# Kernel optimization log

Hardware: AMD Instinct MI355X
Metric: run time of the kernel (lower is better)

## Reference

```python
import jax, jax.numpy as jnp
import numpy as np

B, T, D_IN, H, NH, R = 32, 1024, 64, 128, 4, 3
HD = H // NH  # 32


def _p(key, shape, scale=0.02):
    return jax.random.normal(key, shape, dtype=jnp.float32) * scale


def setup_inputs() -> dict:
    key = jax.random.key(0)
    ks = jax.random.split(key, 8)
    return {
        "x": jax.random.normal(ks[0], (B, T, D_IN), dtype=jnp.float32),
        "theta_w": _p(ks[1], (H, D_IN)),
        "theta_b": jnp.zeros((H,), jnp.float32),
        "in_proj_w": _p(ks[2], (3 * H, H)),
        "in_proj_b": jnp.zeros((3 * H,), jnp.float32),
        "out_proj_w": _p(ks[3], (H, H)),
        "out_proj_b": jnp.zeros((H,), jnp.float32),
        "ln_g": jnp.ones((H,), jnp.float32),
        "ln_b": jnp.zeros((H,), jnp.float32),
        "w1": _p(ks[4], (H, H)),
        "b1": jnp.zeros((H,), jnp.float32),
        "w2": _p(ks[5], (2, H)),
        "b2": jnp.zeros((2,), jnp.float32),
    }


def _build_adj(t, radius):
    # banded adjacency: adj[i,j] = 1/(1+|i-j|) for |i-j| <= radius, row-normalized
    idx = jnp.arange(t)
    d = jnp.abs(idx[:, None] - idx[None, :])
    adj = jnp.where(d <= radius, 1.0 / (1.0 + d.astype(jnp.float32)), 0.0)
    return adj / jnp.clip(adj.sum(axis=1, keepdims=True), 1e-8)


def reference(x, theta_w, theta_b, in_proj_w, in_proj_b, out_proj_w, out_proj_b,
              ln_g, ln_b, w1, b1, w2, b2):
    h = x @ theta_w.T + theta_b                       # [B,T,H]
    adj = _build_adj(T, R)                            # [T,T]
    g = jnp.einsum('ij,bjh->bih', adj, h)             # banded temporal aggregation

    # torch nn.MultiheadAttention (batch_first, eval -> no dropout)
    qkv = g @ in_proj_w.T + in_proj_b                 # [B,T,3H]
    q, k, v = jnp.split(qkv, 3, axis=-1)
    split_heads = lambda t: t.reshape(B, T, NH, HD).transpose(0, 2, 1, 3)
    q, k, v = split_heads(q), split_heads(k), split_heads(v)
    scores = jnp.einsum('bntd,bnsd->bnts', q, k) / jnp.sqrt(jnp.float32(HD))
    attn = jax.nn.softmax(scores, axis=-1)
    o = jnp.einsum('bnts,bnsd->bntd', attn, v)
    o = o.transpose(0, 2, 1, 3).reshape(B, T, H)
    a = o @ out_proj_w.T + out_proj_b                 # [B,T,H]

    # head on last timestep: LayerNorm -> Linear -> GELU(exact) -> Linear
    last = a[:, -1, :]                                # [B,H]
    mu = last.mean(-1, keepdims=True)
    var = ((last - mu) ** 2).mean(-1, keepdims=True)
    ln = (last - mu) / jnp.sqrt(var + 1e-5) * ln_g + ln_b
    hid = jax.nn.gelu(ln @ w1.T + b1, approximate=False)
    return hid @ w2.T + b2                            # [B,2]
```

## Files before the change

### kernel.cpp

```cpp
#include <hip/hip_runtime.h>
#include <math.h>

#define TT 1024

__global__ __launch_bounds__(1024) void k_bn(
    const float* __restrict__ x, const float* __restrict__ theta_w,
    const float* __restrict__ theta_b, const float* __restrict__ ipw,
    const float* __restrict__ ipb, float* __restrict__ u_ws) {
  const int bid = blockIdx.x;
  const int b = bid & 31;
  const int n = bid >> 5;
  const int tid = threadIdx.x;

  __shared__ float s_xs[64];
  __shared__ float s_y[128];
  __shared__ float s_qn[32];
  __shared__ float s_z[128];
  __shared__ __align__(16) float s_r[64];
  __shared__ __align__(16) float s_t[TT];
  __shared__ __align__(16) float s_p[TT];
  __shared__ __align__(16) float s_pt[TT];
  __shared__ float s_up[16][64];
  __shared__ float s_red[16];

  const float* __restrict__ xb = x + (size_t)b * TT * 64;

  if (tid < 64) {
    float acc = xb[(TT - 1) * 64 + tid]
              + 0.5f        * xb[(TT - 2) * 64 + tid]
              + (1.f / 3.f) * xb[(TT - 3) * 64 + tid]
              + 0.25f       * xb[(TT - 4) * 64 + tid];
    s_xs[tid] = acc * (12.f / 25.f);
  }
  __syncthreads();
  if (tid < 128) {
    const float* tr = theta_w + tid * 64;
    float acc = theta_b[tid];
    for (int d = 0; d < 64; ++d) acc += tr[d] * s_xs[d];
    s_y[tid] = acc;
  }
  __syncthreads();
  if (tid < 512) {
    const int g = tid >> 4, l = tid & 15;
    const int e = n * 32 + g;
    const float* wr = ipw + e * 128 + l * 8;
    float acc = 0.f;
    #pragma unroll
    for (int u = 0; u < 8; ++u) acc += wr[u] * s_y[l * 8 + u];
    acc += __shfl_xor(acc, 1);
    acc += __shfl_xor(acc, 2);
    acc += __shfl_xor(acc, 4);
    acc += __shfl_xor(acc, 8);
    if (l == 0) s_qn[g] = acc + ipb[e];
  }
  __syncthreads();
  if (tid < 128) {
    const int c = tid;
    float acc = 0.f;
    for (int e = 0; e < 32; ++e)
      acc += ipw[(128 + n * 32 + e) * 128 + c] * s_qn[e];
    s_z[c] = acc;
  }
  __syncthreads();
  if (tid < 64) {
    const int d = tid;
    float acc = 0.f;
    for (int c = 0; c < 128; ++c) acc += theta_w[c * 64 + d] * s_z[c];
    s_r[d] = acc * 0.17677669529663687f;
  }
  __syncthreads();

  {
    const int g = tid >> 4, l = tid & 15;
    const float4 rv = ((const float4*)s_r)[l];
    for (int it = 0; it < 16; ++it) {
      const int j = it * 64 + g;
      const float4 xv = ((const float4*)(xb + j * 64))[l];
      float p = xv.x * rv.x + xv.y * rv.y + xv.z * rv.z + xv.w * rv.w;
      #pragma unroll
      for (int m = 1; m <= 8; m <<= 1) p += __shfl_xor(p, m);
      if (l == 0) s_t[j] = p;
    }
  }
  __syncthreads();

  {
    const int j = tid;
    float acc = 0.f, wsum = 0.f;
    #pragma unroll
    for (int dj = -3; dj <= 3; ++dj) {
      const int jj = j + dj;
      if (jj >= 0 && jj < TT) {
        const float w = 1.f / (1.f + (float)(dj < 0 ? -dj : dj));
        acc += w * s_t[jj];
        wsum += w;
      }
    }
    const float sc = acc / wsum;
    float lmax = sc;
    #pragma unroll
    for (int m = 32; m >= 1; m >>= 1) lmax = fmaxf(lmax, __shfl_xor(lmax, m));
    if ((tid & 63) == 0) s_red[tid >> 6] = lmax;
    __syncthreads();
    float bmax = -1e30f;
    #pragma unroll
    for (int w = 0; w < 16; ++w) bmax = fmaxf(bmax, s_red[w]);
    __syncthreads();
    const float e = expf(sc - bmax);
    s_p[j] = e / wsum;
    float lsum = e;
    #pragma unroll
    for (int m = 32; m >= 1; m >>= 1) lsum += __shfl_xor(lsum, m);
    if ((tid & 63) == 0) s_red[tid >> 6] = lsum;
    __syncthreads();
    float tsum = 0.f;
    #pragma unroll
    for (int w = 0; w < 16; ++w) tsum += s_red[w];
    const float inv_denom = 1.f / tsum;
    float acc2 = 0.f;
    #pragma unroll
    for (int dj = -3; dj <= 3; ++dj) {
      const int s = j + dj;
      if (s >= 0 && s < TT)
        acc2 += (1.f / (1.f + (float)(dj < 0 ? -dj : dj))) * s_p[s];
    }
    s_pt[j] = acc2 * inv_denom;
  }
  __syncthreads();

  {
    const int jp = tid >> 6, d = tid & 63;
    const float* xr = xb + (size_t)(jp * 64) * 64 + d;
    float acc = 0.f;
    for (int jj = 0; jj < 64; ++jj)
      acc += s_pt[jp * 64 + jj] * xr[jj * 64];
    s_up[jp][d] = acc;
  }
  __syncthreads();
  if (tid < 64) {
    const int d = tid;
    float acc = 0.f;
    for (int c = 0; c < 16; ++c) acc += s_up[c][d];
    u_ws[((size_t)b * 4 + n) * 64 + d] = acc;
  }
}

__global__ __launch_bounds__(128) void k_tail(
    const float* __restrict__ u_in, const float* __restrict__ theta_w,
    const float* __restrict__ theta_b, const float* __restrict__ ipw,
    const float* __restrict__ ipb, const float* __restrict__ Wout,
    const float* __restrict__ outb, const float* __restrict__ ln_g,
    const float* __restrict__ ln_b, const float* __restrict__ w1,
    const float* __restrict__ b1, const float* __restrict__ w2,
    const float* __restrict__ b2, float* __restrict__ out) {
  const int b = blockIdx.x;
  const int tid = threadIdx.x;
  __shared__ float s_u[256];
  __shared__ float s_w[4][128];
  __shared__ float s_o[128], s_ln[128], s_hid[128], s_red[2];

  for (int rep = 0; rep < 2; ++rep) {
    const int idx = tid + rep * 128;
    s_u[idx] = u_in[b * 256 + idx];
  }
  __syncthreads();
  for (int rep = 0; rep < 4; ++rep) {
    const int idx = tid + rep * 128;
    const int n = idx >> 7, c = idx & 127;
    const float* tr = theta_w + c * 64;
    const float* un = &s_u[n * 64];
    float acc = theta_b[c];
    for (int d = 0; d < 64; ++d) acc += tr[d] * un[d];
    s_w[n][c] = acc;
  }
  __syncthreads();
  {
    const int e = tid, n = e >> 5;
    const float* wr = ipw + (256 + e) * 128;
    const float* wn = s_w[n];
    float acc = ipb[256 + e];
    for (int c = 0; c < 128; ++c) acc += wr[c] * wn[c];
    s_o[e] = acc;
  }
  __syncthreads();
  const int e = tid;
  float a = outb[e];
  {
    const float* wr = Wout + e * 128;
    for (int f = 0; f < 128; ++f) a += wr[f] * s_o[f];
  }
  float sum = a;
  #pragma unroll
  for (int m = 32; m >= 1; m >>= 1) sum += __shfl_xor(sum, m);
  if ((e & 63) == 0) s_red[e >> 6] = sum;
  __syncthreads();
  const float mu = (s_red[0] + s_red[1]) * (1.f / 128.f);
  __syncthreads();
  const float d = a - mu;
  float sq = d * d;
  #pragma unroll
  for (int m = 32; m >= 1; m >>= 1) sq += __shfl_xor(sq, m);
  if ((e & 63) == 0) s_red[e >> 6] = sq;
  __syncthreads();
  const float var = (s_red[0] + s_red[1]) * (1.f / 128.f);
  const float ln = d / sqrtf(var + 1e-5f) * ln_g[e] + ln_b[e];
  s_ln[e] = ln;
  __syncthreads();
  float h = b1[e];
  {
    const float* w1r = w1 + e * 128;
    for (int f = 0; f < 128; ++f) h += w1r[f] * s_ln[f];
  }
  h = 0.5f * h * (1.f + erff(h * 0.70710678118654752f));
  s_hid[e] = h;
  __syncthreads();
  if (e < 2) {
    float acc = b2[e];
    const float* w2r = w2 + e * 128;
    for (int f = 0; f < 128; ++f) acc += w2r[f] * s_hid[f];
    out[b * 2 + e] = acc;
  }
}

extern "C" void kernel_launch(void* const* d_in, const int* in_sizes, int n_in,
                              void* d_out, int out_size, void* d_ws, size_t ws_size,
                              hipStream_t stream) {
  const float* x       = (const float*)d_in[0];
  const float* theta_w = (const float*)d_in[1];
  const float* theta_b = (const float*)d_in[2];
  const float* ipw     = (const float*)d_in[3];
  const float* ipb     = (const float*)d_in[4];
  const float* outw    = (const float*)d_in[5];
  const float* outb    = (const float*)d_in[6];
  const float* ln_g    = (const float*)d_in[7];
  const float* ln_b    = (const float*)d_in[8];
  const float* w1      = (const float*)d_in[9];
  const float* b1      = (const float*)d_in[10];
  const float* w2      = (const float*)d_in[11];
  const float* b2      = (const float*)d_in[12];

  float* u_ws = (float*)d_ws;

  k_bn  <<<128, 1024, 0, stream>>>(x, theta_w, theta_b, ipw, ipb, u_ws);
  k_tail<<< 32,  128, 0, stream>>>(u_ws, theta_w, theta_b, ipw, ipb, outw, outb,
                                   ln_g, ln_b, w1, b1, w2, b2, (float*)d_out);
}
```

Measured before the change: 112.3 us.

## Prefetch x rows into registers early, parallelize r reduction, unroll loops

Each thread now loads its 16 float4 slices of x into registers at kernel start, so the global-load latency overlaps the serial chain of small projections instead of being paid after it. The 128-term reduction computing r is split across 512 threads with a partial-sum buffer in shared memory plus a final combine step. Many dot-product loops also get explicit unroll pragmas. In exchange, the register array of 64 floats per thread at 1024 threads per block raises register pressure and may cause spills.

After: 109.2 us. -2.7%, faster.

```diff
diff --git a/kernel.cpp b/kernel.cpp
--- a/kernel.cpp
+++ b/kernel.cpp
@@ -16,6 +16,7 @@
   __shared__ float s_y[128];
   __shared__ float s_qn[32];
   __shared__ float s_z[128];
+  __shared__ float s_rp[8][64];
   __shared__ __align__(16) float s_r[64];
   __shared__ __align__(16) float s_t[TT];
   __shared__ __align__(16) float s_p[TT];
@@ -25,6 +26,12 @@
 
   const float* __restrict__ xb = x + (size_t)b * TT * 64;
 
+  const int g = tid >> 4, l = tid & 15;
+  float4 xv[16];
+  #pragma unroll
+  for (int it = 0; it < 16; ++it)
+    xv[it] = ((const float4*)(xb + (size_t)(it * 64 + g) * 64))[l];
+
   if (tid < 64) {
     float acc = xb[(TT - 1) * 64 + tid]
               + 0.5f        * xb[(TT - 2) * 64 + tid]
@@ -36,47 +43,60 @@
   if (tid < 128) {
     const float* tr = theta_w + tid * 64;
     float acc = theta_b[tid];
+    #pragma unroll 16
     for (int d = 0; d < 64; ++d) acc += tr[d] * s_xs[d];
     s_y[tid] = acc;
   }
   __syncthreads();
   if (tid < 512) {
-    const int g = tid >> 4, l = tid & 15;
-    const int e = n * 32 + g;
-    const float* wr = ipw + e * 128 + l * 8;
-    float acc = 0.f;
-    #pragma unroll
-    for (int u = 0; u < 8; ++u) acc += wr[u] * s_y[l * 8 + u];
+    const int gq = tid >> 4, lq = tid & 15;
+    const int e = n * 32 + gq;
+    const float* wr = ipw + e * 128 + lq * 8;
+    float acc = 0.f;
+    #pragma unroll
+    for (int u = 0; u < 8; ++u) acc += wr[u] * s_y[lq * 8 + u];
     acc += __shfl_xor(acc, 1);
     acc += __shfl_xor(acc, 2);
     acc += __shfl_xor(acc, 4);
     acc += __shfl_xor(acc, 8);
-    if (l == 0) s_qn[g] = acc + ipb[e];
+    if (lq == 0) s_qn[gq] = acc + ipb[e];
   }
   __syncthreads();
   if (tid < 128) {
     const int c = tid;
     float acc = 0.f;
+    #pragma unroll
     for (int e = 0; e < 32; ++e)
       acc += ipw[(128 + n * 32 + e) * 128 + c] * s_qn[e];
     s_z[c] = acc;
   }
   __syncthreads();
+  if (tid < 512) {
+    const int gr = tid >> 6, d = tid & 63;
+    float acc = 0.f;
+    #pragma unroll
+    for (int cc = 0; cc < 16; ++cc) {
+      const int c = gr * 16 + cc;
+      acc += theta_w[c * 64 + d] * s_z[c];
+    }
+    s_rp[gr][d] = acc;
+  }
+  __syncthreads();
   if (tid < 64) {
-    const int d = tid;
-    float acc = 0.f;
-    for (int c = 0; c < 128; ++c) acc += theta_w[c * 64 + d] * s_z[c];
-    s_r[d] = acc * 0.17677669529663687f;
-  }
-  __syncthreads();
-
-  {
-    const int g = tid >> 4, l = tid & 15;
+    float acc = 0.f;
+    #pragma unroll
+    for (int gr = 0; gr < 8; ++gr) acc += s_rp[gr][tid];
+    s_r[tid] = acc * 0.17677669529663687f;
+  }
+  __syncthreads();
+
+  {
     const float4 rv = ((const float4*)s_r)[l];
+    #pragma unroll
     for (int it = 0; it < 16; ++it) {
       const int j = it * 64 + g;
-      const float4 xv = ((const float4*)(xb + j * 64))[l];
-      float p = xv.x * rv.x + xv.y * rv.y + xv.z * rv.z + xv.w * rv.w;
+      const float4 xv4 = xv[it];
+      float p = xv4.x * rv.x + xv4.y * rv.y + xv4.z * rv.z + xv4.w * rv.w;
       #pragma unroll
       for (int m = 1; m <= 8; m <<= 1) p += __shfl_xor(p, m);
       if (l == 0) s_t[j] = p;
@@ -132,6 +152,7 @@
     const int jp = tid >> 6, d = tid & 63;
     const float* xr = xb + (size_t)(jp * 64) * 64 + d;
     float acc = 0.f;
+    #pragma unroll
     for (int jj = 0; jj < 64; ++jj)
       acc += s_pt[jp * 64 + jj] * xr[jj * 64];
     s_up[jp][d] = acc;
@@ -140,6 +161,7 @@
   if (tid < 64) {
     const int d = tid;
     float acc = 0.f;
+    #pragma unroll
     for (int c = 0; c < 16; ++c) acc += s_up[c][d];
     u_ws[((size_t)b * 4 + n) * 64 + d] = acc;
   }
@@ -159,17 +181,20 @@
   __shared__ float s_w[4][128];
   __shared__ float s_o[128], s_ln[128], s_hid[128], s_red[2];
 
+  #pragma unroll
   for (int rep = 0; rep < 2; ++rep) {
     const int idx = tid + rep * 128;
     s_u[idx] = u_in[b * 256 + idx];
   }
   __syncthreads();
+  #pragma unroll
   for (int rep = 0; rep < 4; ++rep) {
     const int idx = tid + rep * 128;
     const int n = idx >> 7, c = idx & 127;
     const float* tr = theta_w + c * 64;
     const float* un = &s_u[n * 64];
     float acc = theta_b[c];
+    #pragma unroll 16
     for (int d = 0; d < 64; ++d) acc += tr[d] * un[d];
     s_w[n][c] = acc;
   }
@@ -179,6 +204,7 @@
     const float* wr = ipw + (256 + e) * 128;
     const float* wn = s_w[n];
     float acc = ipb[256 + e];
+    #pragma unroll 16
     for (int c = 0; c < 128; ++c) acc += wr[c] * wn[c];
     s_o[e] = acc;
   }
@@ -187,6 +213,7 @@
   float a = outb[e];
   {
     const float* wr = Wout + e * 128;
+    #pragma unroll 16
     for (int f = 0; f < 128; ++f) a += wr[f] * s_o[f];
   }
   float sum = a;
@@ -209,6 +236,7 @@
   float h = b1[e];
   {
     const float* w1r = w1 + e * 128;
+    #pragma unroll 16
     for (int f = 0; f < 128; ++f) h += w1r[f] * s_ln[f];
   }
   h = 0.5f * h * (1.f + erff(h * 0.70710678118654752f));
@@ -217,6 +245,7 @@
   if (e < 2) {
     float acc = b2[e];
     const float* w2r = w2 + e * 128;
+    #pragma unroll 16
     for (int f = 0; f < 128; ++f) acc += w2r[f] * s_hid[f];
     out[b * 2 + e] = acc;
   }
```

## Split sequence into chunks per block with all heads, defer softmax normalization

Applied to the files above, without the earlier changes.

Each block now handles a 128-timestep chunk (plus halo) of one batch for all four heads, instead of the full sequence for one head. The x chunk is staged once in shared memory and reused for the score and weighted-sum passes across heads. Softmax drops the max subtraction, so exp is applied to raw scores. Partial sums and exp totals are written to workspace and reduced in the tail kernel. This raises block count and removes block-wide reductions, but risks overflow for large scores and adds workspace traffic.

Result: faster. 109.7 us (-2.3%).

```diff
diff --git a/kernel.cpp b/kernel.cpp
--- a/kernel.cpp
+++ b/kernel.cpp
@@ -3,27 +3,66 @@
 
 #define TT 1024
 
-__global__ __launch_bounds__(1024) void k_bn(
+
+__device__ __forceinline__ void sc_ep(const float* __restrict__ tn,
+                                      float* __restrict__ en,
+                                      float* __restrict__ pn,
+                                      int lr, int jg) {
+  float acc = 0.f, wsum = 0.f;
+  #pragma unroll
+  for (int dj = -3; dj <= 3; ++dj) {
+    const int js = jg + dj;
+    if (js >= 0 && js < TT) {
+      const float w = 1.f / (1.f + (float)(dj < 0 ? -dj : dj));
+      acc += w * tn[lr + dj];
+      wsum += w;
+    }
+  }
+  const float sc = acc / wsum;
+  const float e = expf(sc);
+  en[lr] = e;
+  pn[lr] = e / wsum;
+}
+
+__global__ __launch_bounds__(512) void k_chunk(
     const float* __restrict__ x, const float* __restrict__ theta_w,
     const float* __restrict__ theta_b, const float* __restrict__ ipw,
-    const float* __restrict__ ipb, float* __restrict__ u_ws) {
+    const float* __restrict__ ipb, float* __restrict__ up_ws,
+    float* __restrict__ s_ws) {
   const int bid = blockIdx.x;
   const int b = bid & 31;
-  const int n = bid >> 5;
+  const int c = bid >> 5;
   const int tid = threadIdx.x;
 
+  __shared__ float s_x[144][65];
   __shared__ float s_xs[64];
   __shared__ float s_y[128];
-  __shared__ float s_qn[32];
-  __shared__ float s_z[128];
-  __shared__ __align__(16) float s_r[64];
-  __shared__ __align__(16) float s_t[TT];
-  __shared__ __align__(16) float s_p[TT];
-  __shared__ __align__(16) float s_pt[TT];
-  __shared__ float s_up[16][64];
-  __shared__ float s_red[16];
+  __shared__ float s_q[128];
+  __shared__ float s_z[4][128];
+  __shared__ float s_r[4][64];
+  __shared__ float s_t[4][144];
+  __shared__ float s_e[4][144];
+  __shared__ float s_p[4][144];
+  __shared__ float s_pt[4][128];
+  __shared__ float s_sp[4][2];
 
   const float* __restrict__ xb = x + (size_t)b * TT * 64;
+  const int j0 = c * 128 - 8;
+
+  #pragma unroll
+  for (int k = 0; k < 5; ++k) {
+    const int i4 = tid + k * 512;
+    if (i4 < 144 * 16) {
+      const int lr = i4 >> 4, col = (i4 & 15) * 4;
+      int j = j0 + lr;
+      j = j < 0 ? 0 : (j > TT - 1 ? TT - 1 : j);
+      const float4 v = *(const float4*)(xb + (size_t)j * 64 + col);
+      s_x[lr][col + 0] = v.x;
+      s_x[lr][col + 1] = v.y;
+      s_x[lr][col + 2] = v.z;
+      s_x[lr][col + 3] = v.w;
+    }
+  }
 
   if (tid < 64) {
     float acc = xb[(TT - 1) * 64 + tid]
@@ -36,140 +75,144 @@
   if (tid < 128) {
     const float* tr = theta_w + tid * 64;
     float acc = theta_b[tid];
+    #pragma unroll 16
     for (int d = 0; d < 64; ++d) acc += tr[d] * s_xs[d];
     s_y[tid] = acc;
   }
   __syncthreads();
-  if (tid < 512) {
+  if (tid < 256) {
     const int g = tid >> 4, l = tid & 15;
-    const int e = n * 32 + g;
-    const float* wr = ipw + e * 128 + l * 8;
-    float acc = 0.f;
-    #pragma unroll
-    for (int u = 0; u < 8; ++u) acc += wr[u] * s_y[l * 8 + u];
-    acc += __shfl_xor(acc, 1);
-    acc += __shfl_xor(acc, 2);
-    acc += __shfl_xor(acc, 4);
-    acc += __shfl_xor(acc, 8);
-    if (l == 0) s_qn[g] = acc + ipb[e];
-  }
-  __syncthreads();
-  if (tid < 128) {
-    const int c = tid;
-    float acc = 0.f;
+    for (int pass = 0; pass < 8; ++pass) {
+      const int e = pass * 16 + g;
+      const float* wr = ipw + e * 128 + l * 8;
+      float acc = 0.f;
+      #pragma unroll
+      for (int u = 0; u < 8; ++u) acc += wr[u] * s_y[l * 8 + u];
+      acc += __shfl_xor(acc, 1);
+      acc += __shfl_xor(acc, 2);
+      acc += __shfl_xor(acc, 4);
+      acc += __shfl_xor(acc, 8);
+      if (l == 0) s_q[e] = acc + ipb[e];
+    }
+  }
+  __syncthreads();
+  {
+    const int n = tid >> 7, cc = tid & 127;
+    const float* qn = &s_q[n * 32];
+    float acc = 0.f;
+    #pragma unroll
     for (int e = 0; e < 32; ++e)
-      acc += ipw[(128 + n * 32 + e) * 128 + c] * s_qn[e];
-    s_z[c] = acc;
-  }
-  __syncthreads();
+      acc += ipw[(128 + n * 32 + e) * 128 + cc] * qn[e];
+    s_z[n][cc] = acc;
+  }
+  __syncthreads();
+  if (tid < 256) {
+    const int n = tid >> 6, d = tid & 63;
+    const float* zn = s_z[n];
+    float acc = 0.f;
+    #pragma unroll 16
+    for (int cidx = 0; cidx < 128; ++cidx)
+      acc += theta_w[cidx * 64 + d] * zn[cidx];
+    s_r[n][d] = acc * 0.17677669529663687f;
+  }
+  __syncthreads();
+
+  {
+    const int n = tid >> 7, lr = tid & 127;
+    const float* xr = s_x[lr];
+    const float* rn = s_r[n];
+    float acc = 0.f;
+    #pragma unroll 16
+    for (int d = 0; d < 64; ++d) acc += xr[d] * rn[d];
+    s_t[n][lr] = acc;
+  }
   if (tid < 64) {
-    const int d = tid;
-    float acc = 0.f;
-    for (int c = 0; c < 128; ++c) acc += theta_w[c * 64 + d] * s_z[c];
-    s_r[d] = acc * 0.17677669529663687f;
-  }
-  __syncthreads();
-
-  {
-    const int g = tid >> 4, l = tid & 15;
-    const float4 rv = ((const float4*)s_r)[l];
-    for (int it = 0; it < 16; ++it) {
-      const int j = it * 64 + g;
-      const float4 xv = ((const float4*)(xb + j * 64))[l];
-      float p = xv.x * rv.x + xv.y * rv.y + xv.z * rv.z + xv.w * rv.w;
-      #pragma unroll
-      for (int m = 1; m <= 8; m <<= 1) p += __shfl_xor(p, m);
-      if (l == 0) s_t[j] = p;
-    }
-  }
-  __syncthreads();
-
-  {
-    const int j = tid;
-    float acc = 0.f, wsum = 0.f;
+    const int n = tid >> 4, lr = 128 + (tid & 15);
+    const float* xr = s_x[lr];
+    const float* rn = s_r[n];
+    float acc = 0.f;
+    #pragma unroll 16
+    for (int d = 0; d < 64; ++d) acc += xr[d] * rn[d];
+    s_t[n][lr] = acc;
+  }
+  __syncthreads();
+
+  {
+    const int n = tid >> 7, lr = 5 + (tid & 127);
+    sc_ep(s_t[n], s_e[n], s_p[n], lr, j0 + lr);
+  }
+  if (tid < 24) {
+    const int n = tid / 6, lr = 133 + tid % 6;
+    sc_ep(s_t[n], s_e[n], s_p[n], lr, j0 + lr);
+  }
+  __syncthreads();
+
+  {
+    const int n = tid >> 7, lj = tid & 127;
+    const int lr = 8 + lj, jg = j0 + lr;
+    float acc = 0.f;
     #pragma unroll
     for (int dj = -3; dj <= 3; ++dj) {
-      const int jj = j + dj;
-      if (jj >= 0 && jj < TT) {
-        const float w = 1.f / (1.f + (float)(dj < 0 ? -dj : dj));
-        acc += w * s_t[jj];
-        wsum += w;
-      }
-    }
-    const float sc = acc / wsum;
-    float lmax = sc;
-    #pragma unroll
-    for (int m = 32; m >= 1; m >>= 1) lmax = fmaxf(lmax, __shfl_xor(lmax, m));
-    if ((tid & 63) == 0) s_red[tid >> 6] = lmax;
-    __syncthreads();
-    float bmax = -1e30f;
-    #pragma unroll
-    for (int w = 0; w < 16; ++w) bmax = fmaxf(bmax, s_red[w]);
-    __syncthreads();
-    const float e = expf(sc - bmax);
-    s_p[j] = e / wsum;
-    float lsum = e;
-    #pragma unroll
-    for (int m = 32; m >= 1; m >>= 1) lsum += __shfl_xor(lsum, m);
-    if ((tid & 63) == 0) s_red[tid >> 6] = lsum;
-    __syncthreads();
-    float tsum = 0.f;
-    #pragma unroll
-    for (int w = 0; w < 16; ++w) tsum += s_red[w];
-    const float inv_denom = 1.f / tsum;
-    float acc2 = 0.f;
-    #pragma unroll
-    for (int dj = -3; dj <= 3; ++dj) {
-      const int s = j + dj;
+      const int s = jg + dj;
       if (s >= 0 && s < TT)
-        acc2 += (1.f / (1.f + (float)(dj < 0 ? -dj : dj))) * s_p[s];
-    }
-    s_pt[j] = acc2 * inv_denom;
-  }
-  __syncthreads();
-
-  {
-    const int jp = tid >> 6, d = tid & 63;
-    const float* xr = xb + (size_t)(jp * 64) * 64 + d;
-    float acc = 0.f;
+        acc += (1.f / (1.f + (float)(dj < 0 ? -dj : dj))) * s_p[n][lr + dj];
+    }
+    s_pt[n][lj] = acc;
+    float e = s_e[n][lr];
+    #pragma unroll
+    for (int m = 32; m >= 1; m >>= 1) e += __shfl_xor(e, m);
+    if ((tid & 63) == 0) s_sp[n][(tid >> 6) & 1] = e;
+  }
+  __syncthreads();
+
+  {
+    const int h = tid >> 8, nn = (tid >> 6) & 3, d = tid & 63;
+    float acc = 0.f;
+    #pragma unroll 16
     for (int jj = 0; jj < 64; ++jj)
-      acc += s_pt[jp * 64 + jj] * xr[jj * 64];
-    s_up[jp][d] = acc;
-  }
-  __syncthreads();
-  if (tid < 64) {
-    const int d = tid;
-    float acc = 0.f;
-    for (int c = 0; c < 16; ++c) acc += s_up[c][d];
-    u_ws[((size_t)b * 4 + n) * 64 + d] = acc;
-  }
+      acc += s_pt[nn][h * 64 + jj] * s_x[8 + h * 64 + jj][d];
+    up_ws[((size_t)b * 16 + (c * 2 + h)) * 256 + nn * 64 + d] = acc;
+  }
+  if (tid < 4)
+    s_ws[((size_t)b * 8 + c) * 4 + tid] = s_sp[tid][0] + s_sp[tid][1];
 }
 
 __global__ __launch_bounds__(128) void k_tail(
-    const float* __restrict__ u_in, const float* __restrict__ theta_w,
-    const float* __restrict__ theta_b, const float* __restrict__ ipw,
-    const float* __restrict__ ipb, const float* __restrict__ Wout,
-    const float* __restrict__ outb, const float* __restrict__ ln_g,
-    const float* __restrict__ ln_b, const float* __restrict__ w1,
-    const float* __restrict__ b1, const float* __restrict__ w2,
-    const float* __restrict__ b2, float* __restrict__ out) {
+    const float* __restrict__ up_in, const float* __restrict__ s_in,
+    const float* __restrict__ theta_w, const float* __restrict__ theta_b,
+    const float* __restrict__ ipw, const float* __restrict__ ipb,
+    const float* __restrict__ Wout, const float* __restrict__ outb,
+    const float* __restrict__ ln_g, const float* __restrict__ ln_b,
+    const float* __restrict__ w1, const float* __restrict__ b1,
+    const float* __restrict__ w2, const float* __restrict__ b2,
+    float* __restrict__ out) {
   const int b = blockIdx.x;
   const int tid = threadIdx.x;
   __shared__ float s_u[256];
   __shared__ float s_w[4][128];
   __shared__ float s_o[128], s_ln[128], s_hid[128], s_red[2];
 
+  #pragma unroll
   for (int rep = 0; rep < 2; ++rep) {
     const int idx = tid + rep * 128;
-    s_u[idx] = u_in[b * 256 + idx];
-  }
-  __syncthreads();
+    const int n = idx >> 6;
+    float acc = 0.f;
+    #pragma unroll
+    for (int cc = 0; cc < 16; ++cc) acc += up_in[(b * 16 + cc) * 256 + idx];
+    float S = 0.f;
+    #pragma unroll
+    for (int cc = 0; cc < 8; ++cc) S += s_in[(b * 8 + cc) * 4 + n];
+    s_u[idx] = acc / S;
+  }
+  __syncthreads();
+  #pragma unroll
   for (int rep = 0; rep < 4; ++rep) {
     const int idx = tid + rep * 128;
     const int n = idx >> 7, c = idx & 127;
     const float* tr = theta_w + c * 64;
     const float* un = &s_u[n * 64];
     float acc = theta_b[c];
+    #pragma unroll 16
     for (int d = 0; d < 64; ++d) acc += tr[d] * un[d];
     s_w[n][c] = acc;
   }
@@ -179,6 +222,7 @@
     const float* wr = ipw + (256 + e) * 128;
     const float* wn = s_w[n];
     float acc = ipb[256 + e];
+    #pragma unroll 16
     for (int c = 0; c < 128; ++c) acc += wr[c] * wn[c];
     s_o[e] = acc;
   }
@@ -187,6 +231,7 @@
   float a = outb[e];
   {
     const float* wr = Wout + e * 128;
+    #pragma unroll 16
     for (int f = 0; f < 128; ++f) a += wr[f] * s_o[f];
   }
   float sum = a;
@@ -209,6 +254,7 @@
   float h = b1[e];
   {
     const float* w1r = w1 + e * 128;
+    #pragma unroll 16
     for (int f = 0; f < 128; ++f) h += w1r[f] * s_ln[f];
   }
   h = 0.5f * h * (1.f + erff(h * 0.70710678118654752f));
@@ -217,6 +263,7 @@
   if (e < 2) {
     float acc = b2[e];
     const float* w2r = w2 + e * 128;
+    #pragma unroll 16
     for (int f = 0; f < 128; ++f) acc += w2r[f] * s_hid[f];
     out[b * 2 + e] = acc;
   }
@@ -239,9 +286,11 @@
   const float* w2      = (const float*)d_in[11];
   const float* b2      = (const float*)d_in[12];
 
-  float* u_ws = (float*)d_ws;
-
-  k_bn  <<<128, 1024, 0, stream>>>(x, theta_w, theta_b, ipw, ipb, u_ws);
-  k_tail<<< 32,  128, 0, stream>>>(u_ws, theta_w, theta_b, ipw, ipb, outw, outb,
-                                   ln_g, ln_b, w1, b1, w2, b2, (float*)d_out);
-}
+  float* up_ws = (float*)d_ws;
+  float* s_ws  = (float*)d_ws + 131072;
+
+  k_chunk<<<256, 512, 0, stream>>>(x, theta_w, theta_b, ipw, ipb, up_ws, s_ws);
+  k_tail <<< 32, 128, 0, stream>>>(up_ws, s_ws, theta_w, theta_b, ipw, ipb,
+                                   outw, outb, ln_g, ln_b, w1, b1, w2, b2,
+                                   (float*)d_out);
+}
```
